# Kernel tuning notes

Measured on AMD Instinct MI355X. Metric: run time of the kernel, lower is better.

The kernel has to match this reference:

```python
import jax, jax.numpy as jnp
import numpy as np

EPS = 1e-05
GROUPS = 8


def setup_inputs() -> dict:
    key = jax.random.key(0)
    k1, k2, k3 = jax.random.split(key, 3)
    N, C, H, W = 32, 256, 56, 56
    x = jax.random.normal(k1, (N, C, H, W), dtype=jnp.float32)
    weight = jnp.ones((C,), dtype=jnp.float32)
    bias = jnp.zeros((C,), dtype=jnp.float32)
    gate_logits = jnp.array([2.8, 0.2, 1.1], dtype=jnp.float32)
    diag_proj = jnp.array([[0.08, -0.05, 0.08],
                           [-0.03, 0.08, -0.01],
                           [-0.05, -0.04, -0.07]], dtype=jnp.float32)
    return {"x": x, "weight": weight, "bias": bias,
            "gate_logits": gate_logits, "diag_proj": diag_proj}


def reference(x, weight, bias, gate_logits, diag_proj):
    xf = x.astype(jnp.float32)
    N, C, H, W = xf.shape

    # variance descriptor (differentiable: first-instance path recomputes without detach)
    batch_var = jnp.var(xf, axis=(0, 2, 3)).mean()    # per-channel var -> mean
    sample_var = jnp.var(xf, axis=(1, 2, 3)).mean()   # per-sample var -> mean
    channel_var = jnp.var(xf, axis=1).mean()          # var over channels at each (n,h,w) -> mean
    desc = jnp.tanh(jnp.log(jnp.maximum(jnp.stack([batch_var, sample_var, channel_var]), EPS)))

    gate = jax.nn.softmax(gate_logits + diag_proj @ desc)  # [3]

    # batch norm (training mode: batch statistics over N,H,W per channel)
    mu_b = xf.mean(axis=(0, 2, 3), keepdims=True)
    var_b = xf.var(axis=(0, 2, 3), keepdims=True)
    x_bn = (xf - mu_b) / jnp.sqrt(var_b + EPS)

    # layer norm = group_norm with 1 group: per-sample stats over C,H,W
    mu_l = xf.mean(axis=(1, 2, 3), keepdims=True)
    var_l = xf.var(axis=(1, 2, 3), keepdims=True)
    x_ln = (xf - mu_l) / jnp.sqrt(var_l + EPS)

    # group norm with GROUPS groups
    xg = xf.reshape(N, GROUPS, C // GROUPS, H, W)
    mu_g = xg.mean(axis=(2, 3, 4), keepdims=True)
    var_g = xg.var(axis=(2, 3, 4), keepdims=True)
    x_gn = ((xg - mu_g) / jnp.sqrt(var_g + EPS)).reshape(N, C, H, W)

    mixed = gate[0] * x_bn + gate[1] * x_ln + gate[2] * x_gn
    y = mixed * weight[None, :, None, None] + bias[None, :, None, None]
    return y.astype(x.dtype)
```

## Files before the change

kernel.cpp:

```cpp
#include <hip/hip_runtime.h>
#include <hip/hip_bf16.h>

#define NN 32
#define CC 256
#define HW 3136
#define HW4 784
#define CHW 802816
#define CHW4 200704
#define NCHW 25690112
#define GROUPS 8
#define CPG 32
#define NHW 100352
#define GHW 100352
#define EPSF 1e-5f

#define PB16 49
#define NSTAT (NN*PB16)
#define NPT2 NSTAT

typedef float f32x4 __attribute__((ext_vector_type(4)));

__global__ __launch_bounds__(256) void stats_kernel(
    const float4* __restrict__ x4,
    float2* __restrict__ S12p,
    float* __restrict__ pT2)
{
    const int bx = blockIdx.x;
    const int n = bx / PB16, pb = bx - n * PB16;
    const int tid = threadIdx.x;
    const int w = tid >> 6, lane = tid & 63;
    const int cl = lane >> 3;
    const int pl = lane & 7;
    const int P0 = pb * 16;

    const float4* base = x4 + (size_t)n * CHW4 + P0 + pl;

    float s1a[8], s2a[8];
    float4 T0 = make_float4(0.f, 0.f, 0.f, 0.f);
    float4 T1 = make_float4(0.f, 0.f, 0.f, 0.f);
    #pragma unroll
    for (int k = 0; k < 8; ++k) {
        const int c = (k * 4 + w) * 8 + cl;
        float4 v0 = base[(size_t)c * HW4];
        float4 v1 = base[(size_t)c * HW4 + 8];
        T0.x += v0.x; T0.y += v0.y; T0.z += v0.z; T0.w += v0.w;
        T1.x += v1.x; T1.y += v1.y; T1.z += v1.z; T1.w += v1.w;
        s1a[k] = v0.x + v0.y + v0.z + v0.w + v1.x + v1.y + v1.z + v1.w;
        s2a[k] = v0.x*v0.x + v0.y*v0.y + v0.z*v0.z + v0.w*v0.w
               + v1.x*v1.x + v1.y*v1.y + v1.z*v1.z + v1.w*v1.w;
    }

    #pragma unroll
    for (int k = 0; k < 8; ++k) {
        #pragma unroll
        for (int off = 1; off < 8; off <<= 1) {
            s1a[k] += __shfl_down(s1a[k], off, 64);
            s2a[k] += __shfl_down(s2a[k], off, 64);
        }
    }
    if (pl == 0) {
        #pragma unroll
        for (int k = 0; k < 8; ++k) {
            const int c = (k * 4 + w) * 8 + cl;
            S12p[(size_t)bx * 256 + c] = make_float2(s1a[k], s2a[k]);
        }
    }

    #pragma unroll
    for (int off = 8; off < 64; off <<= 1) {
        T0.x += __shfl_xor(T0.x, off, 64);
        T0.y += __shfl_xor(T0.y, off, 64);
        T0.z += __shfl_xor(T0.z, off, 64);
        T0.w += __shfl_xor(T0.w, off, 64);
        T1.x += __shfl_xor(T1.x, off, 64);
        T1.y += __shfl_xor(T1.y, off, 64);
        T1.z += __shfl_xor(T1.z, off, 64);
        T1.w += __shfl_xor(T1.w, off, 64);
    }
    __shared__ float4 shT[4][16];
    if (lane < 8) {
        shT[w][pl] = T0;
        shT[w][8 + pl] = T1;
    }
    __syncthreads();
    if (tid < 16) {
        float4 a = shT[0][tid], b = shT[1][tid], c4 = shT[2][tid], d = shT[3][tid];
        const float tx = a.x + b.x + c4.x + d.x;
        const float ty = a.y + b.y + c4.y + d.y;
        const float tz = a.z + b.z + c4.z + d.z;
        const float tw = a.w + b.w + c4.w + d.w;
        float t2 = tx*tx + ty*ty + tz*tz + tw*tw;
        #pragma unroll
        for (int off = 1; off < 16; off <<= 1) t2 += __shfl_down(t2, off, 64);
        if (tid == 0) pT2[bx] = t2;
    }
}

__global__ __launch_bounds__(256) void fold_kernel(
    const float2* __restrict__ S12p, float2* __restrict__ S12)
{
    const int n = blockIdx.x, c = threadIdx.x;
    const float2* p = S12p + (size_t)n * PB16 * 256 + c;
    float a = 0.f, b = 0.f;
    #pragma unroll 7
    for (int pb = 0; pb < PB16; ++pb) {
        float2 v = p[(size_t)pb * 256];
        a += v.x; b += v.y;
    }
    S12[n * 256 + c] = make_float2(a, b);
}

__global__ __launch_bounds__(256) void finalize_kernel(
    const float2* __restrict__ S12, const float* __restrict__ partialT2,
    const float* __restrict__ gate_logits, const float* __restrict__ diag_proj,
    float2* __restrict__ CB, float2* __restrict__ CL, float2* __restrict__ CG,
    float* __restrict__ GT)
{
    const int tid = threadIdx.x;
    __shared__ float sh_red1[4], sh_red2[4], sh_red3[4], sh_red4[4];

    const float inv_NHW  = 1.f / (float)NHW;
    const float inv_CHW  = 1.f / (float)CHW;
    const float inv_GHW  = 1.f / (float)GHW;
    const float inv_NCHW = 1.f / (float)NCHW;

    const int c = tid;
    float s1 = 0.f, s2 = 0.f;
    for (int n = 0; n < NN; ++n) {
        float2 v = S12[n * CC + c];
        s1 += v.x; s2 += v.y;
    }
    const float mu_b  = s1 * inv_NHW;
    const float var_b = s2 * inv_NHW - mu_b * mu_b;
    CB[c] = make_float2(mu_b, rsqrtf(var_b + EPSF));

    const int ng_n = tid >> 3, ng_g = tid & 7;
    float s1g = 0.f, s2g = 0.f;
    for (int cc2 = 0; cc2 < CPG; ++cc2) {
        float2 v = S12[ng_n * CC + ng_g * CPG + cc2];
        s1g += v.x; s2g += v.y;
    }
    const float mu_g  = s1g * inv_GHW;
    const float var_g = s2g * inv_GHW - mu_g * mu_g;
    CG[tid] = make_float2(mu_g, rsqrtf(var_g + EPSF));

    float s1l = s1g, s2l = s2g;
    #pragma unroll
    for (int off = 1; off < 8; off <<= 1) {
        s1l += __shfl_xor(s1l, off, 64);
        s2l += __shfl_xor(s2l, off, 64);
    }
    float var_l_contrib = 0.f;
    if (ng_g == 0) {
        const float mu_l  = s1l * inv_CHW;
        const float var_l = s2l * inv_CHW - mu_l * mu_l;
        CL[ng_n] = make_float2(mu_l, rsqrtf(var_l + EPSF));
        var_l_contrib = var_l;
    }

    float t2p = 0.f;
    for (int i = tid; i < NPT2; i += 256) t2p += partialT2[i];

    float r1 = var_b, r2 = s2, r3 = var_l_contrib, r4 = t2p;
    #pragma unroll
    for (int off = 32; off; off >>= 1) {
        r1 += __shfl_down(r1, off, 64);
        r2 += __shfl_down(r2, off, 64);
        r3 += __shfl_down(r3, off, 64);
        r4 += __shfl_down(r4, off, 64);
    }
    const int wave = tid >> 6, lane = tid & 63;
    if (lane == 0) { sh_red1[wave] = r1; sh_red2[wave] = r2; sh_red3[wave] = r3; sh_red4[wave] = r4; }
    __syncthreads();
    if (tid == 0) {
        const float sum_var_b = sh_red1[0] + sh_red1[1] + sh_red1[2] + sh_red1[3];
        const float total_x2  = sh_red2[0] + sh_red2[1] + sh_red2[2] + sh_red2[3];
        const float sum_var_l = sh_red3[0] + sh_red3[1] + sh_red3[2] + sh_red3[3];
        const float sum_T2    = sh_red4[0] + sh_red4[1] + sh_red4[2] + sh_red4[3];

        const float batch_var   = sum_var_b * (1.f / (float)CC);
        const float sample_var  = sum_var_l * (1.f / (float)NN);
        const float channel_var = total_x2 * inv_NCHW
                                - sum_T2 * inv_NHW * (1.f / ((float)CC * (float)CC));

        float desc[3];
        desc[0] = tanhf(logf(fmaxf(batch_var,   EPSF)));
        desc[1] = tanhf(logf(fmaxf(sample_var,  EPSF)));
        desc[2] = tanhf(logf(fmaxf(channel_var, EPSF)));

        float lg[3];
        #pragma unroll
        for (int i = 0; i < 3; ++i) {
            lg[i] = gate_logits[i] + diag_proj[i*3+0]*desc[0]
                                   + diag_proj[i*3+1]*desc[1]
                                   + diag_proj[i*3+2]*desc[2];
        }
        const float m = fmaxf(lg[0], fmaxf(lg[1], lg[2]));
        const float e0 = expf(lg[0]-m), e1 = expf(lg[1]-m), e2 = expf(lg[2]-m);
        const float inv = 1.f / (e0 + e1 + e2);
        GT[0] = e0 * inv; GT[1] = e1 * inv; GT[2] = e2 * inv;
    }
}

__global__ __launch_bounds__(256) void apply_kernel(
    const f32x4* __restrict__ x4,
    const float* __restrict__ weight, const float* __restrict__ bias,
    const float2* __restrict__ CB, const float2* __restrict__ CL,
    const float2* __restrict__ CG, const float* __restrict__ GT,
    f32x4* __restrict__ y4)
{
    const int nc = blockIdx.x;
    const int n = nc >> 8, ch = nc & 255, g = ch >> 5;
    const float g0 = GT[0], g1 = GT[1], g2 = GT[2];
    const float2 cb = CB[ch], cl2 = CL[n], cg2 = CG[n * 8 + g];
    const float w = weight[ch], bi = bias[ch];
    const float scale = g0 * cb.y + g1 * cl2.y + g2 * cg2.y;
    const float offs  = g0 * cb.x * cb.y + g1 * cl2.x * cl2.y + g2 * cg2.x * cg2.y;
    const float a = w * scale;
    const float b = fmaf(-w, offs, bi);

    const f32x4* xp = x4 + (size_t)nc * HW4;
    f32x4* yp = y4 + (size_t)nc * HW4;
    const int tid = threadIdx.x;

    f32x4 v0 = xp[tid];
    f32x4 v1 = xp[tid + 256];
    f32x4 v2 = xp[tid + 512];
    f32x4 v3;
    if (tid < 16) v3 = xp[tid + 768];

    f32x4 r0, r1, r2, r3;
    r0.x = fmaf(v0.x, a, b); r0.y = fmaf(v0.y, a, b); r0.z = fmaf(v0.z, a, b); r0.w = fmaf(v0.w, a, b);
    r1.x = fmaf(v1.x, a, b); r1.y = fmaf(v1.y, a, b); r1.z = fmaf(v1.z, a, b); r1.w = fmaf(v1.w, a, b);
    r2.x = fmaf(v2.x, a, b); r2.y = fmaf(v2.y, a, b); r2.z = fmaf(v2.z, a, b); r2.w = fmaf(v2.w, a, b);
    __builtin_nontemporal_store(r0, &yp[tid]);
    __builtin_nontemporal_store(r1, &yp[tid + 256]);
    __builtin_nontemporal_store(r2, &yp[tid + 512]);
    if (tid < 16) {
        r3.x = fmaf(v3.x, a, b); r3.y = fmaf(v3.y, a, b); r3.z = fmaf(v3.z, a, b); r3.w = fmaf(v3.w, a, b);
        __builtin_nontemporal_store(r3, &yp[tid + 768]);
    }
}

extern "C" void kernel_launch(void* const* d_in, const int* in_sizes, int n_in,
                              void* d_out, int out_size, void* d_ws, size_t ws_size,
                              hipStream_t stream) {
    const float* x           = (const float*)d_in[0];
    const float* weight      = (const float*)d_in[1];
    const float* bias        = (const float*)d_in[2];
    const float* gate_logits = (const float*)d_in[3];
    const float* diag_proj   = (const float*)d_in[4];
    float* out = (float*)d_out;

    float* ws   = (float*)d_ws;
    float2* S12p = (float2*)ws;
    float2* S12  = (float2*)(ws + 802816);
    float2* CB   = (float2*)(ws + 819200);
    float2* CL   = (float2*)(ws + 819712);
    float2* CG   = (float2*)(ws + 819776);
    float*  GT   = ws + 820288;
    float*  pT2  = ws + 820296;

    stats_kernel<<<NSTAT, 256, 0, stream>>>((const float4*)x, S12p, pT2);
    fold_kernel<<<NN, 256, 0, stream>>>(S12p, S12);
    finalize_kernel<<<1, 256, 0, stream>>>(S12, pT2, gate_logits, diag_proj,
                                           CB, CL, CG, GT);
    apply_kernel<<<NN * CC, 256, 0, stream>>>((const f32x4*)x, weight, bias,
                                              CB, CL, CG, GT, (f32x4*)out);
}
```

Measured before the change: 62.82 us.

## Fuse fold and finalize via last-block ticket; process two channels per apply block

```diff
diff --git a/kernel.cpp b/kernel.cpp
--- a/kernel.cpp
+++ b/kernel.cpp
@@ -96,27 +96,38 @@
     }
 }
 
-__global__ __launch_bounds__(256) void fold_kernel(
-    const float2* __restrict__ S12p, float2* __restrict__ S12)
-{
-    const int n = blockIdx.x, c = threadIdx.x;
-    const float2* p = S12p + (size_t)n * PB16 * 256 + c;
-    float a = 0.f, b = 0.f;
-    #pragma unroll 7
-    for (int pb = 0; pb < PB16; ++pb) {
-        float2 v = p[(size_t)pb * 256];
-        a += v.x; b += v.y;
-    }
-    S12[n * 256 + c] = make_float2(a, b);
-}
-
-__global__ __launch_bounds__(256) void finalize_kernel(
-    const float2* __restrict__ S12, const float* __restrict__ partialT2,
+__global__ __launch_bounds__(256) void fold_finalize_kernel(
+    const float2* __restrict__ S12p, const float* __restrict__ partialT2,
     const float* __restrict__ gate_logits, const float* __restrict__ diag_proj,
+    float2* __restrict__ S12,
     float2* __restrict__ CB, float2* __restrict__ CL, float2* __restrict__ CG,
-    float* __restrict__ GT)
+    float* __restrict__ GT, unsigned* ticket)
 {
     const int tid = threadIdx.x;
+
+    {
+        const int n = blockIdx.x;
+        const float2* p = S12p + (size_t)n * PB16 * 256 + tid;
+        float a = 0.f, b = 0.f;
+        #pragma unroll 7
+        for (int pb = 0; pb < PB16; ++pb) {
+            float2 v = p[(size_t)pb * 256];
+            a += v.x; b += v.y;
+        }
+        S12[n * 256 + tid] = make_float2(a, b);
+    }
+
+    __shared__ bool sh_last;
+    __syncthreads();
+    if (tid == 0) {
+        __threadfence();
+        unsigned old = atomicAdd(ticket, 1u);
+        sh_last = (old == NN - 1u);
+    }
+    __syncthreads();
+    if (!sh_last) return;
+    __threadfence();
+
     __shared__ float sh_red1[4], sh_red2[4], sh_red3[4], sh_red4[4];
 
     const float inv_NHW  = 1.f / (float)NHW;
@@ -209,36 +220,54 @@
     const float2* __restrict__ CG, const float* __restrict__ GT,
     f32x4* __restrict__ y4)
 {
-    const int nc = blockIdx.x;
-    const int n = nc >> 8, ch = nc & 255, g = ch >> 5;
+    const int nc0 = blockIdx.x * 2, nc1 = nc0 + 1;
     const float g0 = GT[0], g1 = GT[1], g2 = GT[2];
-    const float2 cb = CB[ch], cl2 = CL[n], cg2 = CG[n * 8 + g];
-    const float w = weight[ch], bi = bias[ch];
-    const float scale = g0 * cb.y + g1 * cl2.y + g2 * cg2.y;
-    const float offs  = g0 * cb.x * cb.y + g1 * cl2.x * cl2.y + g2 * cg2.x * cg2.y;
-    const float a = w * scale;
-    const float b = fmaf(-w, offs, bi);
-
-    const f32x4* xp = x4 + (size_t)nc * HW4;
-    f32x4* yp = y4 + (size_t)nc * HW4;
+
+    const int n0 = nc0 >> 8, ch0 = nc0 & 255, gg0 = ch0 >> 5;
+    const float2 cb0 = CB[ch0], cl0 = CL[n0], cg0 = CG[n0 * 8 + gg0];
+    const float w0 = weight[ch0], bi0 = bias[ch0];
+    const float a0 = w0 * (g0 * cb0.y + g1 * cl0.y + g2 * cg0.y);
+    const float b0 = fmaf(-w0, g0 * cb0.x * cb0.y + g1 * cl0.x * cl0.y + g2 * cg0.x * cg0.y, bi0);
+
+    const int n1 = nc1 >> 8, ch1 = nc1 & 255, gg1 = ch1 >> 5;
+    const float2 cb1 = CB[ch1], cl1 = CL[n1], cg1 = CG[n1 * 8 + gg1];
+    const float w1 = weight[ch1], bi1 = bias[ch1];
+    const float a1 = w1 * (g0 * cb1.y + g1 * cl1.y + g2 * cg1.y);
+    const float b1 = fmaf(-w1, g0 * cb1.x * cb1.y + g1 * cl1.x * cl1.y + g2 * cg1.x * cg1.y, bi1);
+
+    const f32x4* xp0 = x4 + (size_t)nc0 * HW4;
+    const f32x4* xp1 = x4 + (size_t)nc1 * HW4;
+    f32x4* yp0 = y4 + (size_t)nc0 * HW4;
+    f32x4* yp1 = y4 + (size_t)nc1 * HW4;
     const int tid = threadIdx.x;
 
-    f32x4 v0 = xp[tid];
-    f32x4 v1 = xp[tid + 256];
-    f32x4 v2 = xp[tid + 512];
-    f32x4 v3;
-    if (tid < 16) v3 = xp[tid + 768];
-
-    f32x4 r0, r1, r2, r3;
-    r0.x = fmaf(v0.x, a, b); r0.y = fmaf(v0.y, a, b); r0.z = fmaf(v0.z, a, b); r0.w = fmaf(v0.w, a, b);
-    r1.x = fmaf(v1.x, a, b); r1.y = fmaf(v1.y, a, b); r1.z = fmaf(v1.z, a, b); r1.w = fmaf(v1.w, a, b);
-    r2.x = fmaf(v2.x, a, b); r2.y = fmaf(v2.y, a, b); r2.z = fmaf(v2.z, a, b); r2.w = fmaf(v2.w, a, b);
-    __builtin_nontemporal_store(r0, &yp[tid]);
-    __builtin_nontemporal_store(r1, &yp[tid + 256]);
-    __builtin_nontemporal_store(r2, &yp[tid + 512]);
+    f32x4 u0 = xp0[tid];
+    f32x4 u1 = xp0[tid + 256];
+    f32x4 u2 = xp0[tid + 512];
+    f32x4 v0 = xp1[tid];
+    f32x4 v1 = xp1[tid + 256];
+    f32x4 v2 = xp1[tid + 512];
+    f32x4 u3, v3;
+    if (tid < 16) { u3 = xp0[tid + 768]; v3 = xp1[tid + 768]; }
+
+    f32x4 r;
+    r.x = fmaf(u0.x, a0, b0); r.y = fmaf(u0.y, a0, b0); r.z = fmaf(u0.z, a0, b0); r.w = fmaf(u0.w, a0, b0);
+    __builtin_nontemporal_store(r, &yp0[tid]);
+    r.x = fmaf(u1.x, a0, b0); r.y = fmaf(u1.y, a0, b0); r.z = fmaf(u1.z, a0, b0); r.w = fmaf(u1.w, a0, b0);
+    __builtin_nontemporal_store(r, &yp0[tid + 256]);
+    r.x = fmaf(u2.x, a0, b0); r.y = fmaf(u2.y, a0, b0); r.z = fmaf(u2.z, a0, b0); r.w = fmaf(u2.w, a0, b0);
+    __builtin_nontemporal_store(r, &yp0[tid + 512]);
+    r.x = fmaf(v0.x, a1, b1); r.y = fmaf(v0.y, a1, b1); r.z = fmaf(v0.z, a1, b1); r.w = fmaf(v0.w, a1, b1);
+    __builtin_nontemporal_store(r, &yp1[tid]);
+    r.x = fmaf(v1.x, a1, b1); r.y = fmaf(v1.y, a1, b1); r.z = fmaf(v1.z, a1, b1); r.w = fmaf(v1.w, a1, b1);
+    __builtin_nontemporal_store(r, &yp1[tid + 256]);
+    r.x = fmaf(v2.x, a1, b1); r.y = fmaf(v2.y, a1, b1); r.z = fmaf(v2.z, a1, b1); r.w = fmaf(v2.w, a1, b1);
+    __builtin_nontemporal_store(r, &yp1[tid + 512]);
     if (tid < 16) {
-        r3.x = fmaf(v3.x, a, b); r3.y = fmaf(v3.y, a, b); r3.z = fmaf(v3.z, a, b); r3.w = fmaf(v3.w, a, b);
-        __builtin_nontemporal_store(r3, &yp[tid + 768]);
+        r.x = fmaf(u3.x, a0, b0); r.y = fmaf(u3.y, a0, b0); r.z = fmaf(u3.z, a0, b0); r.w = fmaf(u3.w, a0, b0);
+        __builtin_nontemporal_store(r, &yp0[tid + 768]);
+        r.x = fmaf(v3.x, a1, b1); r.y = fmaf(v3.y, a1, b1); r.z = fmaf(v3.z, a1, b1); r.w = fmaf(v3.w, a1, b1);
+        __builtin_nontemporal_store(r, &yp1[tid + 768]);
     }
 }
 
@@ -260,11 +289,13 @@
     float2* CG   = (float2*)(ws + 819776);
     float*  GT   = ws + 820288;
     float*  pT2  = ws + 820296;
+    unsigned* ticket = (unsigned*)(ws + 821888);
+
+    hipMemsetAsync(ticket, 0, sizeof(unsigned), stream);
 
     stats_kernel<<<NSTAT, 256, 0, stream>>>((const float4*)x, S12p, pT2);
-    fold_kernel<<<NN, 256, 0, stream>>>(S12p, S12);
-    finalize_kernel<<<1, 256, 0, stream>>>(S12, pT2, gate_logits, diag_proj,
-                                           CB, CL, CG, GT);
-    apply_kernel<<<NN * CC, 256, 0, stream>>>((const f32x4*)x, weight, bias,
-                                              CB, CL, CG, GT, (f32x4*)out);
+    fold_finalize_kernel<<<NN, 256, 0, stream>>>(S12p, pT2, gate_logits, diag_proj,
+                                                 S12, CB, CL, CG, GT, ticket);
+    apply_kernel<<<NN * CC / 2, 256, 0, stream>>>((const f32x4*)x, weight, bias,
+                                                  CB, CL, CG, GT, (f32x4*)out);
 }
```

After: 68.66 us. +9.3%, slower.
